# Optimization experiments

Measured on AMD Instinct MI355X. Metric: run time of the kernel, lower is better.

## Reference

```python
import jax, jax.numpy as jnp
import numpy as np

B, ENC_LEN, DEC_LEN = 4, 1024, 256
ENC_H, DEC_H, ATTN = 1024, 1024, 256


def setup_inputs() -> dict:
    key = jax.random.key(0)
    k1, k2, k3, k4, k5, k6 = jax.random.split(key, 6)
    scale = 0.02
    return {
        "encoded_seq": jax.random.normal(k1, (B, ENC_LEN, ENC_H), jnp.float32),
        "decoder_state": jax.random.normal(k2, (B, DEC_LEN, DEC_H), jnp.float32),
        "input_pad_mask": jnp.ones((B, ENC_LEN), jnp.float32),
        "Wh": jax.random.normal(k3, (ENC_H, ATTN), jnp.float32) * scale,
        "Ws": jax.random.normal(k4, (DEC_H, ATTN), jnp.float32) * scale,
        "bs": jax.random.normal(k5, (ATTN,), jnp.float32) * scale,
        "v": jax.random.normal(k6, (ATTN,), jnp.float32) * scale,
    }


def reference(encoded_seq, decoder_state, input_pad_mask, Wh, Ws, bs, v):
    # projections: [B, dec, A] and [B, enc, A]
    proj_dec = jnp.einsum('bdh,ha->bda', decoder_state, Ws) + bs
    proj_enc = jnp.einsum('beh,ha->bea', encoded_seq, Wh)
    # additive score: tanh(broadcast add) then dot with selector vector v
    added = jnp.tanh(proj_dec[:, :, None, :] + proj_enc[:, None, :, :])  # [B,dec,enc,A]
    attn_logits = jnp.einsum('bdea,a->bde', added, v)                    # [B,dec,enc]
    attn_weights = jax.nn.softmax(attn_logits, axis=-1)
    attn_weights2 = attn_weights * input_pad_mask[:, None, :]
    attn_renorm = attn_weights2 / jnp.sum(attn_weights2, axis=-1, keepdims=True)
    context = jnp.einsum('bde,beh->bdh', attn_renorm, encoded_seq)       # [B,dec,enc_h]
    return context, attn_renorm
```

## Files before the change

### kernel.cpp

```cpp
#include <hip/hip_runtime.h>
#include <hip/hip_bf16.h>

#define BB 4
#define ENC_LEN 1024
#define DEC_LEN 256
#define ENC_H 1024
#define ATTN_A 256

#define C2F 2.8853900817779268f

typedef short bf16x8 __attribute__((ext_vector_type(8)));
typedef float f32x4 __attribute__((ext_vector_type(4)));
typedef unsigned int u32x2 __attribute__((ext_vector_type(2)));

union Q2D {
  uint4 q;
  u32x2 d[2];
};
union BF8 {
  u32x2 d[2];
  bf16x8 v;
};

static __device__ __forceinline__ unsigned short f2bf(float x) {
  union {
    float f;
    unsigned int u;
  } c;
  c.f = x;
  unsigned int r = c.u + 0x7FFFu + ((c.u >> 16) & 1u);
  return (unsigned short)(r >> 16);
}

__global__ __launch_bounds__(256) void prep_k(
    const float* __restrict__ Wh, const float* __restrict__ Ws,
    const float* __restrict__ enc, const float* __restrict__ dec,
    unsigned short* __restrict__ WhT, unsigned short* __restrict__ WsT,
    unsigned short* __restrict__ encT, unsigned short* __restrict__ encB,
    unsigned short* __restrict__ decB) {
  __shared__ unsigned short T[64][68];
  const int wb = blockIdx.x;
  const int t = threadIdx.x;
  const int lr = t >> 4;
  const int lc4 = (t & 15) * 4;

  if (wb >= 1152) {
    const int q = wb - 1152;
    const int r0 = (q >> 4) * 64;
    const int c0 = (q & 15) * 64;
#pragma unroll
    for (int p = 0; p < 4; ++p) {
      const int r = lr + p * 16;
      const float4 v = *(const float4*)&dec[(long)(r0 + r) * ENC_H + c0 + lc4];
      ushort4 o;
      o.x = f2bf(v.x);
      o.y = f2bf(v.y);
      o.z = f2bf(v.z);
      o.w = f2bf(v.w);
      *(ushort4*)&decB[(long)(r0 + r) * ENC_H + c0 + lc4] = o;
    }
    return;
  }

  const float* in;
  unsigned short* out;
  unsigned short* out2 = nullptr;
  int R, C, bx, by;
  if (wb < 128) {
    in = (wb < 64) ? Wh : Ws;
    out = (wb < 64) ? WhT : WsT;
    const int tt = wb & 63;
    R = ENC_H;
    C = ATTN_A;
    bx = tt & 3;
    by = tt >> 2;
  } else {
    const int tt0 = wb - 128;
    const int b = tt0 >> 8;
    const int tt = tt0 & 255;
    in = enc + (long)b * ENC_LEN * ENC_H;
    out = encT + (long)b * ENC_H * ENC_LEN;
    out2 = encB + (long)b * ENC_LEN * ENC_H;
    R = ENC_LEN;
    C = ENC_H;
    bx = tt & 15;
    by = tt >> 4;
  }
  const int r0 = by * 64;
  const int c0 = bx * 64;

#pragma unroll
  for (int p = 0; p < 4; ++p) {
    const int r = lr + p * 16;
    const float4 v = *(const float4*)&in[(long)(r0 + r) * C + c0 + lc4];
    ushort4 o;
    o.x = f2bf(v.x);
    o.y = f2bf(v.y);
    o.z = f2bf(v.z);
    o.w = f2bf(v.w);
    *(ushort4*)&T[r][lc4] = o;
    if (out2) *(ushort4*)&out2[(long)(r0 + r) * C + c0 + lc4] = o;
  }
  __syncthreads();
#pragma unroll
  for (int p = 0; p < 4; ++p) {
    const int c = lr + p * 16;
    ushort4 o;
    o.x = T[lc4 + 0][c];
    o.y = T[lc4 + 1][c];
    o.z = T[lc4 + 2][c];
    o.w = T[lc4 + 3][c];
    *(ushort4*)&out[(long)(c0 + c) * R + r0 + lc4] = o;
  }
}

__global__ __launch_bounds__(256) void pgemm(const unsigned short* __restrict__ decB,
                                             const unsigned short* __restrict__ encB,
                                             const unsigned short* __restrict__ WsT,
                                             const unsigned short* __restrict__ WhT,
                                             float* __restrict__ pdP,
                                             float* __restrict__ peP) {
  __shared__ unsigned short As[64][36];
  __shared__ unsigned short Bs[64][36];
  __shared__ float Cs[64][68];

  const int s = blockIdx.z;
  const bool isPD = blockIdx.y < 16;
  const unsigned short* A = isPD ? decB : encB;
  const unsigned short* BT = isPD ? WsT : WhT;
  const int m0 = (isPD ? blockIdx.y : (blockIdx.y - 16)) * 64;
  const int n0 = blockIdx.x * 64;
  const int kb = s * 512;

  const int tid = threadIdx.x;
  const int lane = tid & 63;
  const int wave = tid >> 6;
  const int quad = lane >> 4;
  const int l16 = lane & 15;
  const int wm = (wave >> 1) * 32;
  const int wn = (wave & 1) * 32;
  const int sr = tid >> 2;
  const int sk = (tid & 3) * 8;

  f32x4 acc[2][2] = {{{0.f, 0.f, 0.f, 0.f}, {0.f, 0.f, 0.f, 0.f}},
                     {{0.f, 0.f, 0.f, 0.f}, {0.f, 0.f, 0.f, 0.f}}};

  const unsigned short* Ap = A + (long)(m0 + sr) * ENC_H + kb + sk;
  const unsigned short* Bp = BT + (long)(n0 + sr) * ENC_H + kb + sk;

  Q2D av, bv;
  av.q = *(const uint4*)(Ap);
  bv.q = *(const uint4*)(Bp);

  for (int k0 = 0; k0 < 512; k0 += 32) {
    __syncthreads();
    *(u32x2*)&As[sr][sk] = av.d[0];
    *(u32x2*)&As[sr][sk + 4] = av.d[1];
    *(u32x2*)&Bs[sr][sk] = bv.d[0];
    *(u32x2*)&Bs[sr][sk + 4] = bv.d[1];
    const int kn = (k0 + 32 < 512) ? (k0 + 32) : 0;
    av.q = *(const uint4*)(Ap + kn);
    bv.q = *(const uint4*)(Bp + kn);
    __syncthreads();

    bf16x8 af[2], bfr[2];
#pragma unroll
    for (int i = 0; i < 2; ++i) {
      BF8 t;
      t.d[0] = *(const u32x2*)&As[wm + i * 16 + l16][quad * 8];
      t.d[1] = *(const u32x2*)&As[wm + i * 16 + l16][quad * 8 + 4];
      af[i] = t.v;
    }
#pragma unroll
    for (int j = 0; j < 2; ++j) {
      BF8 t;
      t.d[0] = *(const u32x2*)&Bs[wn + j * 16 + l16][quad * 8];
      t.d[1] = *(const u32x2*)&Bs[wn + j * 16 + l16][quad * 8 + 4];
      bfr[j] = t.v;
    }
#pragma unroll
    for (int i = 0; i < 2; ++i)
#pragma unroll
      for (int j = 0; j < 2; ++j)
        acc[i][j] = __builtin_amdgcn_mfma_f32_16x16x32_bf16(af[i], bfr[j], acc[i][j],
                                                            0, 0, 0);
  }

  if (isPD) {
    float* out = pdP + (long)s * (1024 * ATTN_A);
#pragma unroll
    for (int j = 0; j < 2; ++j) {
      const int col = n0 + wn + j * 16 + l16;
#pragma unroll
      for (int i = 0; i < 2; ++i) {
        const int row = m0 + wm + i * 16 + quad * 4;
#pragma unroll
        for (int r = 0; r < 4; ++r)
          out[(long)(row + r) * ATTN_A + col] = C2F * acc[i][j][r];
      }
    }
  } else {
    __syncthreads();
#pragma unroll
    for (int i = 0; i < 2; ++i)
#pragma unroll
      for (int j = 0; j < 2; ++j)
#pragma unroll
        for (int r = 0; r < 4; ++r)
          Cs[wn + j * 16 + l16][wm + i * 16 + quad * 4 + r] = C2F * acc[i][j][r];
    __syncthreads();
    const int gb = m0 >> 10;
    const int e0 = m0 & 1023;
    float* out = peP + (long)s * (BB * ATTN_A * ENC_LEN);
#pragma unroll
    for (int p = 0; p < 4; ++p) {
      const int arow = (tid >> 4) + p * 16;
      const int e4 = (tid & 15) * 4;
      const float4 o = *(const float4*)&Cs[arow][e4];
      *(float4*)&out[(long)gb * (ATTN_A * ENC_LEN) + (long)(n0 + arow) * ENC_LEN +
                     e0 + e4] = o;
    }
  }
}

__global__ __launch_bounds__(256) void logits_k(const float* __restrict__ peP,
                                                const float* __restrict__ pdP,
                                                const float* __restrict__ v,
                                                const float* __restrict__ bs,
                                                float* __restrict__ p0,
                                                float* __restrict__ p1) {
  const int tid = threadIdx.x;
  const int e = blockIdx.x * 256 + tid;
  const int d0 = blockIdx.y * 8;
  const int b = blockIdx.z >> 1;
  const int a0 = (blockIdx.z & 1) * 128;

  __shared__ float Ed[128][8];
  __shared__ float vv[128];

  if (tid < 128) {
    const float cb = C2F * bs[a0 + tid];
#pragma unroll
    for (int dd = 0; dd < 8; ++dd) {
      const long idx = (long)(b * DEC_LEN + d0 + dd) * ATTN_A + a0 + tid;
      const float t = pdP[idx] + pdP[idx + 1024 * ATTN_A] + cb;
      Ed[tid][dd] = __builtin_amdgcn_exp2f(t);
    }
    vv[tid] = -2.0f * v[a0 + tid];
  }
  __syncthreads();

  float acc[8] = {0.f, 0.f, 0.f, 0.f, 0.f, 0.f, 0.f, 0.f};
  const float* pe0 = peP + (long)b * (ATTN_A * ENC_LEN) + (long)a0 * ENC_LEN + e;
  const float* pe1 = pe0 + (long)BB * ATTN_A * ENC_LEN;

  float pn0[4], pn1[4];
#pragma unroll
  for (int u = 0; u < 4; ++u) {
    pn0[u] = pe0[(long)u * ENC_LEN];
    pn1[u] = pe1[(long)u * ENC_LEN];
  }

  for (int a4 = 0; a4 < 128; a4 += 4) {
    float Ee[4];
#pragma unroll
    for (int u = 0; u < 4; ++u) Ee[u] = __builtin_amdgcn_exp2f(pn0[u] + pn1[u]);
    const int an = (a4 + 4 < 128) ? (a4 + 4) : 0;
#pragma unroll
    for (int u = 0; u < 4; ++u) {
      pn0[u] = pe0[(long)(an + u) * ENC_LEN];
      pn1[u] = pe1[(long)(an + u) * ENC_LEN];
    }
    const float4 v4 = *(const float4*)&vv[a4];

    float ed[4][8];
#pragma unroll
    for (int u = 0; u < 4; ++u) {
      const float4 e0v = *(const float4*)&Ed[a4 + u][0];
      const float4 e1v = *(const float4*)&Ed[a4 + u][4];
      ed[u][0] = e0v.x;
      ed[u][1] = e0v.y;
      ed[u][2] = e0v.z;
      ed[u][3] = e0v.w;
      ed[u][4] = e1v.x;
      ed[u][5] = e1v.y;
      ed[u][6] = e1v.z;
      ed[u][7] = e1v.w;
    }

#pragma unroll
    for (int dd = 0; dd < 8; ++dd) {
      const float dn0 = fmaf(ed[0][dd], Ee[0], 1.0f);
      const float dn1 = fmaf(ed[1][dd], Ee[1], 1.0f);
      const float dn2 = fmaf(ed[2][dd], Ee[2], 1.0f);
      const float dn3 = fmaf(ed[3][dd], Ee[3], 1.0f);
      const float x12 = dn0 * dn1;
      const float x34 = dn2 * dn3;
      float t1 = v4.x * dn1;
      t1 = fmaf(v4.y, dn0, t1);
      float t2 = v4.z * dn3;
      t2 = fmaf(v4.w, dn2, t2);
      float num = t1 * x34;
      num = fmaf(t2, x12, num);
      const float D = x12 * x34;
      const float r = __builtin_amdgcn_rcpf(D);
      acc[dd] = fmaf(num, r, acc[dd]);
    }
  }

  float* po = (blockIdx.z & 1) ? p1 : p0;
  const long base = ((long)(b * DEC_LEN + d0) * ENC_LEN) + e;
#pragma unroll
  for (int dd = 0; dd < 8; ++dd) po[base + (long)dd * ENC_LEN] = acc[dd];
}

__global__ __launch_bounds__(256) void softmax2_k(float* __restrict__ p0,
                                                  const float* __restrict__ p1,
                                                  const float* __restrict__ mask,
                                                  unsigned short* __restrict__ attnB) {
  const int row = blockIdx.x;
  const int b = row >> 8;
  const int tid = threadIdx.x;
  float* rp = p0 + (long)row * ENC_LEN;
  const float* rq = p1 + (long)row * ENC_LEN;
  const float* mp = mask + b * ENC_LEN;
  unsigned short* rb = attnB + (long)row * ENC_LEN;

  float l[4], m[4];
#pragma unroll
  for (int j = 0; j < 4; ++j) {
    l[j] = rp[tid + 256 * j] + rq[tid + 256 * j];
    m[j] = mp[tid + 256 * j];
  }

  __shared__ float redmax[4];
  __shared__ float redsum[4];
  const int lane = tid & 63;
  const int wid = tid >> 6;

  float tm = fmaxf(fmaxf(l[0], l[1]), fmaxf(l[2], l[3]));
#pragma unroll
  for (int off = 1; off < 64; off <<= 1) tm = fmaxf(tm, __shfl_xor(tm, off, 64));
  if (lane == 0) redmax[wid] = tm;
  __syncthreads();
  const float rmax = fmaxf(fmaxf(redmax[0], redmax[1]), fmaxf(redmax[2], redmax[3]));

  const float LOG2E = 1.4426950408889634f;
  float p[4];
  float ts = 0.f;
#pragma unroll
  for (int j = 0; j < 4; ++j) {
    p[j] = __builtin_amdgcn_exp2f((l[j] - rmax) * LOG2E) * m[j];
    ts += p[j];
  }
#pragma unroll
  for (int off = 1; off < 64; off <<= 1) ts += __shfl_xor(ts, off, 64);
  if (lane == 0) redsum[wid] = ts;
  __syncthreads();
  const float rsum = redsum[0] + redsum[1] + redsum[2] + redsum[3];

  const float inv = 1.0f / rsum;
#pragma unroll
  for (int j = 0; j < 4; ++j) {
    const float w = p[j] * inv;
    rp[tid + 256 * j] = w;
    rb[tid + 256 * j] = f2bf(w);
  }
}

__global__ __launch_bounds__(256) void cgemm(const unsigned short* __restrict__ attnB,
                                             const unsigned short* __restrict__ encT,
                                             float* __restrict__ cP) {
  __shared__ unsigned short As[64][36];
  __shared__ unsigned short Bs[64][36];

  const int b = blockIdx.z >> 1;
  const int s = blockIdx.z & 1;
  const int kb = s * 512;
  const unsigned short* A = attnB + (long)b * DEC_LEN * ENC_LEN;
  const unsigned short* BT = encT + (long)b * ENC_H * ENC_LEN;
  float* C = cP + (long)s * (BB * DEC_LEN * ENC_H) + (long)b * DEC_LEN * ENC_H;

  const int tid = threadIdx.x;
  const int lane = tid & 63;
  const int wave = tid >> 6;
  const int quad = lane >> 4;
  const int l16 = lane & 15;
  const int wm = (wave >> 1) * 32;
  const int wn = (wave & 1) * 32;
  const int m0 = blockIdx.y * 64;
  const int n0 = blockIdx.x * 64;
  const int sr = tid >> 2;
  const int sk = (tid & 3) * 8;

  f32x4 acc[2][2] = {{{0.f, 0.f, 0.f, 0.f}, {0.f, 0.f, 0.f, 0.f}},
                     {{0.f, 0.f, 0.f, 0.f}, {0.f, 0.f, 0.f, 0.f}}};

  const unsigned short* Ap = A + (long)(m0 + sr) * ENC_LEN + kb + sk;
  const unsigned short* Bp = BT + (long)(n0 + sr) * ENC_LEN + kb + sk;

  Q2D av, bv;
  av.q = *(const uint4*)(Ap);
  bv.q = *(const uint4*)(Bp);

  for (int k0 = 0; k0 < 512; k0 += 32) {
    __syncthreads();
    *(u32x2*)&As[sr][sk] = av.d[0];
    *(u32x2*)&As[sr][sk + 4] = av.d[1];
    *(u32x2*)&Bs[sr][sk] = bv.d[0];
    *(u32x2*)&Bs[sr][sk + 4] = bv.d[1];
    const int kn = (k0 + 32 < 512) ? (k0 + 32) : 0;
    av.q = *(const uint4*)(Ap + kn);
    bv.q = *(const uint4*)(Bp + kn);
    __syncthreads();

    bf16x8 af[2], bfr[2];
#pragma unroll
    for (int i = 0; i < 2; ++i) {
      BF8 t;
      t.d[0] = *(const u32x2*)&As[wm + i * 16 + l16][quad * 8];
      t.d[1] = *(const u32x2*)&As[wm + i * 16 + l16][quad * 8 + 4];
      af[i] = t.v;
    }
#pragma unroll
    for (int j = 0; j < 2; ++j) {
      BF8 t;
      t.d[0] = *(const u32x2*)&Bs[wn + j * 16 + l16][quad * 8];
      t.d[1] = *(const u32x2*)&Bs[wn + j * 16 + l16][quad * 8 + 4];
      bfr[j] = t.v;
    }
#pragma unroll
    for (int i = 0; i < 2; ++i)
#pragma unroll
      for (int j = 0; j < 2; ++j)
        acc[i][j] = __builtin_amdgcn_mfma_f32_16x16x32_bf16(af[i], bfr[j], acc[i][j],
                                                            0, 0, 0);
  }

#pragma unroll
  for (int j = 0; j < 2; ++j) {
    const int col = n0 + wn + j * 16 + l16;
#pragma unroll
    for (int i = 0; i < 2; ++i) {
      const int row = m0 + wm + i * 16 + quad * 4;
#pragma unroll
      for (int r = 0; r < 4; ++r) C[(long)(row + r) * ENC_H + col] = acc[i][j][r];
    }
  }
}

__global__ __launch_bounds__(256) void creduce(const float* __restrict__ cP,
                                               float* __restrict__ ctx) {
  const long i = ((long)blockIdx.x * 256 + threadIdx.x) * 4;
  const float4 x = *(const float4*)&cP[i];
  const float4 y = *(const float4*)&cP[i + (long)BB * DEC_LEN * ENC_H];
  float4 o;
  o.x = x.x + y.x;
  o.y = x.y + y.y;
  o.z = x.z + y.z;
  o.w = x.w + y.w;
  *(float4*)&ctx[i] = o;
}

template <int OMODE, bool BIAS>
__global__ __launch_bounds__(256) void gemm64(const float* __restrict__ A,
                                              const float* __restrict__ B,
                                              const float* __restrict__ bias,
                                              float* __restrict__ C,
                                              int K, int lda, int ldb, int ldc,
                                              long sA, long sB, long sC) {
  const int bz = blockIdx.z;
  A += (long)bz * sA;
  B += (long)bz * sB;
  C += (long)bz * sC;

  const int tid = threadIdx.x;
  const int tx = tid & 15;
  const int ty = tid >> 4;

  __shared__ float As2[16][64];
  __shared__ float Bs2[16][64];

  float acc[4][4];
#pragma unroll
  for (int i = 0; i < 4; ++i)
#pragma unroll
    for (int j = 0; j < 4; ++j) acc[i][j] = 0.f;

  const int ar = tid >> 2;
  const int ak4 = (tid & 3) << 2;
  const int br = tid >> 4;
  const int bn4 = (tid & 15) << 2;

  const float* Aload = A + (long)(blockIdx.y * 64 + ar) * lda + ak4;
  const float* Bload = B + (long)br * ldb + blockIdx.x * 64 + bn4;

  for (int k0 = 0; k0 < K; k0 += 16) {
    const float4 av = *(const float4*)(Aload + k0);
    const float4 bv = *(const float4*)(Bload + (long)k0 * ldb);
    __syncthreads();
    As2[ak4 + 0][ar] = av.x;
    As2[ak4 + 1][ar] = av.y;
    As2[ak4 + 2][ar] = av.z;
    As2[ak4 + 3][ar] = av.w;
    *(float4*)&Bs2[br][bn4] = bv;
    __syncthreads();
#pragma unroll
    for (int kk = 0; kk < 16; ++kk) {
      const float4 a4 = *(const float4*)&As2[kk][ty << 2];
      const float4 b4 = *(const float4*)&Bs2[kk][tx << 2];
      const float am[4] = {a4.x, a4.y, a4.z, a4.w};
      const float bn[4] = {b4.x, b4.y, b4.z, b4.w};
#pragma unroll
      for (int i = 0; i < 4; ++i)
#pragma unroll
        for (int j = 0; j < 4; ++j) acc[i][j] = fmaf(am[i], bn[j], acc[i][j]);
    }
  }

  if (OMODE == 0) {
    const int row0 = blockIdx.y * 64 + (ty << 2);
    const int col0 = blockIdx.x * 64 + (tx << 2);
    float4 bb4 = make_float4(0.f, 0.f, 0.f, 0.f);
    if (BIAS) bb4 = *(const float4*)&bias[col0];
#pragma unroll
    for (int i = 0; i < 4; ++i) {
      float4 o;
      o.x = acc[i][0] + bb4.x;
      o.y = acc[i][1] + bb4.y;
      o.z = acc[i][2] + bb4.z;
      o.w = acc[i][3] + bb4.w;
      *(float4*)&C[(long)(row0 + i) * ldc + col0] = o;
    }
  } else {
#pragma unroll
    for (int i = 0; i < 4; ++i) {
      const int gr = blockIdx.y * 64 + (ty << 2) + i;
      const int b = gr >> 10;
      const int e = gr & 1023;
#pragma unroll
      for (int j = 0; j < 4; ++j) {
        const int col = blockIdx.x * 64 + (tx << 2) + j;
        C[(long)b * (ATTN_A * ENC_LEN) + (long)col * ENC_LEN + e] = acc[i][j];
      }
    }
  }
}

__global__ __launch_bounds__(256) void logits_fb(const float* __restrict__ peT,
                                                 const float* __restrict__ pd,
                                                 const float* __restrict__ v,
                                                 float* __restrict__ out) {
  const int tid = threadIdx.x;
  const int e = blockIdx.x * 256 + tid;
  const int d0 = blockIdx.y * 8;
  const int b = blockIdx.z;

  __shared__ float cpd[ATTN_A][8];
  __shared__ float vv[ATTN_A];

  {
    const int a = tid;
#pragma unroll
    for (int dd = 0; dd < 8; ++dd)
      cpd[a][dd] = C2F * pd[((b * DEC_LEN + d0 + dd) * ATTN_A) + a];
    vv[a] = -2.0f * v[a];
  }
  __syncthreads();

  float acc[8] = {0.f, 0.f, 0.f, 0.f, 0.f, 0.f, 0.f, 0.f};
  const float* pe = peT + (long)b * (ATTN_A * ENC_LEN) + e;

  for (int a = 0; a < ATTN_A; a += 4) {
    float pes[4];
#pragma unroll
    for (int u = 0; u < 4; ++u) pes[u] = pe[(long)(a + u) * ENC_LEN];
#pragma unroll
    for (int u = 0; u < 4; ++u) {
      const float cpe = C2F * pes[u];
      const float vu = vv[a + u];
      const float4 c0 = *(const float4*)&cpd[a + u][0];
      const float4 c1 = *(const float4*)&cpd[a + u][4];
      const float cd[8] = {c0.x, c0.y, c0.z, c0.w, c1.x, c1.y, c1.z, c1.w};
#pragma unroll
      for (int dd = 0; dd < 8; ++dd) {
        const float x = cd[dd] + cpe;
        const float ex = __builtin_amdgcn_exp2f(x);
        const float r = __builtin_amdgcn_rcpf(ex + 1.0f);
        acc[dd] = fmaf(vu, r, acc[dd]);
      }
    }
  }

  const long base = ((long)(b * DEC_LEN + d0) * ENC_LEN) + e;
#pragma unroll
  for (int dd = 0; dd < 8; ++dd) out[base + (long)dd * ENC_LEN] = acc[dd];
}

__global__ __launch_bounds__(256) void softmax_fb(float* __restrict__ attn,
                                                  const float* __restrict__ mask) {
  const int row = blockIdx.x;
  const int b = row >> 8;
  const int tid = threadIdx.x;
  float* rp = attn + (long)row * ENC_LEN;
  const float* mp = mask + b * ENC_LEN;

  float l[4], m[4];
#pragma unroll
  for (int j = 0; j < 4; ++j) {
    l[j] = rp[tid + 256 * j];
    m[j] = mp[tid + 256 * j];
  }

  __shared__ float redmax[4];
  __shared__ float redsum[4];
  const int lane = tid & 63;
  const int wid = tid >> 6;

  float tm = fmaxf(fmaxf(l[0], l[1]), fmaxf(l[2], l[3]));
#pragma unroll
  for (int off = 1; off < 64; off <<= 1) tm = fmaxf(tm, __shfl_xor(tm, off, 64));
  if (lane == 0) redmax[wid] = tm;
  __syncthreads();
  const float rmax = fmaxf(fmaxf(redmax[0], redmax[1]), fmaxf(redmax[2], redmax[3]));

  const float LOG2E = 1.4426950408889634f;
  float p[4];
  float ts = 0.f;
#pragma unroll
  for (int j = 0; j < 4; ++j) {
    p[j] = __builtin_amdgcn_exp2f((l[j] - rmax) * LOG2E) * m[j];
    ts += p[j];
  }
#pragma unroll
  for (int off = 1; off < 64; off <<= 1) ts += __shfl_xor(ts, off, 64);
  if (lane == 0) redsum[wid] = ts;
  __syncthreads();
  const float rsum = redsum[0] + redsum[1] + redsum[2] + redsum[3];

  const float inv = 1.0f / rsum;
#pragma unroll
  for (int j = 0; j < 4; ++j) rp[tid + 256 * j] = p[j] * inv;
}

extern "C" void kernel_launch(void* const* d_in, const int* in_sizes, int n_in,
                              void* d_out, int out_size, void* d_ws, size_t ws_size,
                              hipStream_t stream) {
  const float* enc = (const float*)d_in[0];
  const float* dec = (const float*)d_in[1];
  const float* mask = (const float*)d_in[2];
  const float* Wh = (const float*)d_in[3];
  const float* Ws = (const float*)d_in[4];
  const float* bs = (const float*)d_in[5];
  const float* v = (const float*)d_in[6];

  float* ctx = (float*)d_out;
  float* attn = ctx + (long)BB * DEC_LEN * ENC_H;

  const long N_PD = 2L * 1024 * ATTN_A;
  const long N_PE = 2L * BB * ATTN_A * ENC_LEN;
  const long N_P1 = (long)BB * DEC_LEN * ENC_LEN;
  const long N_CP = 2L * BB * DEC_LEN * ENC_H;
  const long N_ENC = (long)BB * ENC_H * ENC_LEN;
  const long N_W = (long)ATTN_A * ENC_H;
  const long N_DEC = 1024L * ENC_H;
  const long N_ATT = (long)BB * DEC_LEN * ENC_LEN;
  const size_t FAST_WS = (N_PD + N_PE + N_P1 + N_CP) * 4 +
                         (N_ENC + 2 * N_W + N_ENC + N_DEC + N_ATT) * 2;

  if (ws_size >= FAST_WS) {
    float* pdP = (float*)d_ws;
    float* peP = pdP + N_PD;
    float* p1 = peP + N_PE;
    float* cP = p1 + N_P1;
    unsigned short* encT = (unsigned short*)(cP + N_CP);
    unsigned short* WhT = encT + N_ENC;
    unsigned short* WsT = WhT + N_W;
    unsigned short* encB = WsT + N_W;
    unsigned short* decB = encB + N_ENC;
    unsigned short* attnB = decB + N_DEC;

    prep_k<<<dim3(1408, 1, 1), 256, 0, stream>>>(Wh, Ws, enc, dec, WhT, WsT, encT,
                                                 encB, decB);
    pgemm<<<dim3(4, 80, 2), 256, 0, stream>>>(decB, encB, WsT, WhT, pdP, peP);
    logits_k<<<dim3(4, 32, BB * 2), 256, 0, stream>>>(peP, pdP, v, bs, attn, p1);
    softmax2_k<<<dim3(BB * DEC_LEN, 1, 1), 256, 0, stream>>>(attn, p1, mask, attnB);
    cgemm<<<dim3(16, 4, BB * 2), 256, 0, stream>>>(attnB, encT, cP);
    creduce<<<dim3(1024, 1, 1), 256, 0, stream>>>(cP, ctx);
  } else {
    float* pd = (float*)d_ws;
    float* peT = pd + (long)BB * DEC_LEN * ATTN_A;

    gemm64<0, true><<<dim3(ATTN_A / 64, (BB * DEC_LEN) / 64, 1), 256, 0, stream>>>(
        dec, Ws, bs, pd, ENC_H, ENC_H, ATTN_A, ATTN_A, 0, 0, 0);
    gemm64<1, false><<<dim3(ATTN_A / 64, (BB * ENC_LEN) / 64, 1), 256, 0, stream>>>(
        enc, Wh, nullptr, peT, ENC_H, ENC_H, ATTN_A, 0, 0, 0, 0);
    logits_fb<<<dim3(ENC_LEN / 256, DEC_LEN / 8, BB), 256, 0, stream>>>(peT, pd, v,
                                                                        attn);
    softmax_fb<<<dim3(BB * DEC_LEN, 1, 1), 256, 0, stream>>>(attn, mask);
    gemm64<0, false><<<dim3(ENC_H / 64, DEC_LEN / 64, BB), 256, 0, stream>>>(
        attn, enc, nullptr, ctx, ENC_LEN, ENC_LEN, ENC_H, ENC_H,
        (long)DEC_LEN * ENC_LEN, (long)ENC_LEN * ENC_H, (long)DEC_LEN * ENC_H);
  }
}
```

Before: 141.3 us.

## Drop split-K partials; fuse exp2 and bias into projection GEMM epilogue

The projection GEMM and the context GEMM no longer split K in two. This removes the partial-sum buffers, the creduce kernel and the extra partial read in softmax. The projection GEMM epilogue now applies the bias and exp2 directly and writes transposed enc exponentials straight from the MFMA layout, so logits_k no longer recomputes exp per (d, a) pair. logits_k now handles all 256 attention dims per block with an 8-way product-of-denominators trick, which means fewer rcp calls. The cost is fewer blocks (half the parallelism in both GEMMs) and longer K loops. The larger product of eight denominators also risks overflow.

```diff
diff --git a/kernel.cpp b/kernel.cpp
--- a/kernel.cpp
+++ b/kernel.cpp
@@ -118,19 +118,36 @@
                                              const unsigned short* __restrict__ encB,
                                              const unsigned short* __restrict__ WsT,
                                              const unsigned short* __restrict__ WhT,
-                                             float* __restrict__ pdP,
-                                             float* __restrict__ peP) {
+                                             const float* __restrict__ bs,
+                                             float* __restrict__ Ed,
+                                             float* __restrict__ Ee) {
   __shared__ unsigned short As[64][36];
   __shared__ unsigned short Bs[64][36];
-  __shared__ float Cs[64][68];
-
-  const int s = blockIdx.z;
-  const bool isPD = blockIdx.y < 16;
-  const unsigned short* A = isPD ? decB : encB;
-  const unsigned short* BT = isPD ? WsT : WhT;
-  const int m0 = (isPD ? blockIdx.y : (blockIdx.y - 16)) * 64;
-  const int n0 = blockIdx.x * 64;
-  const int kb = s * 512;
+
+  const int bid = blockIdx.x;
+  const bool isPD = bid < 64;
+  const unsigned short* A;
+  const unsigned short* BT;
+  float* out;
+  int ldc, m0, n0;
+  if (isPD) {
+    A = decB;
+    BT = WsT;
+    out = Ed;
+    ldc = ATTN_A;
+    m0 = (bid >> 2) * 64;
+    n0 = (bid & 3) * 64;
+  } else {
+    const int q = bid - 64;
+    const int b = q >> 6;
+    const int r = q & 63;
+    A = WhT;
+    BT = encB + (long)b * ENC_LEN * ENC_H;
+    out = Ee + (long)b * ATTN_A * ENC_LEN;
+    ldc = ENC_LEN;
+    m0 = (r >> 4) * 64;
+    n0 = (r & 15) * 64;
+  }
 
   const int tid = threadIdx.x;
   const int lane = tid & 63;
@@ -145,20 +162,20 @@
   f32x4 acc[2][2] = {{{0.f, 0.f, 0.f, 0.f}, {0.f, 0.f, 0.f, 0.f}},
                      {{0.f, 0.f, 0.f, 0.f}, {0.f, 0.f, 0.f, 0.f}}};
 
-  const unsigned short* Ap = A + (long)(m0 + sr) * ENC_H + kb + sk;
-  const unsigned short* Bp = BT + (long)(n0 + sr) * ENC_H + kb + sk;
+  const unsigned short* Ap = A + (long)(m0 + sr) * ENC_H + sk;
+  const unsigned short* Bp = BT + (long)(n0 + sr) * ENC_H + sk;
 
   Q2D av, bv;
   av.q = *(const uint4*)(Ap);
   bv.q = *(const uint4*)(Bp);
 
-  for (int k0 = 0; k0 < 512; k0 += 32) {
+  for (int k0 = 0; k0 < 1024; k0 += 32) {
     __syncthreads();
     *(u32x2*)&As[sr][sk] = av.d[0];
     *(u32x2*)&As[sr][sk + 4] = av.d[1];
     *(u32x2*)&Bs[sr][sk] = bv.d[0];
     *(u32x2*)&Bs[sr][sk + 4] = bv.d[1];
-    const int kn = (k0 + 32 < 512) ? (k0 + 32) : 0;
+    const int kn = (k0 + 32 < 1024) ? (k0 + 32) : 0;
     av.q = *(const uint4*)(Ap + kn);
     bv.q = *(const uint4*)(Bp + kn);
     __syncthreads();
@@ -186,150 +203,113 @@
                                                             0, 0, 0);
   }
 
-  if (isPD) {
-    float* out = pdP + (long)s * (1024 * ATTN_A);
-#pragma unroll
-    for (int j = 0; j < 2; ++j) {
-      const int col = n0 + wn + j * 16 + l16;
-#pragma unroll
-      for (int i = 0; i < 2; ++i) {
-        const int row = m0 + wm + i * 16 + quad * 4;
-#pragma unroll
-        for (int r = 0; r < 4; ++r)
-          out[(long)(row + r) * ATTN_A + col] = C2F * acc[i][j][r];
-      }
-    }
-  } else {
-    __syncthreads();
-#pragma unroll
-    for (int i = 0; i < 2; ++i)
-#pragma unroll
-      for (int j = 0; j < 2; ++j)
-#pragma unroll
-        for (int r = 0; r < 4; ++r)
-          Cs[wn + j * 16 + l16][wm + i * 16 + quad * 4 + r] = C2F * acc[i][j][r];
-    __syncthreads();
-    const int gb = m0 >> 10;
-    const int e0 = m0 & 1023;
-    float* out = peP + (long)s * (BB * ATTN_A * ENC_LEN);
-#pragma unroll
-    for (int p = 0; p < 4; ++p) {
-      const int arow = (tid >> 4) + p * 16;
-      const int e4 = (tid & 15) * 4;
-      const float4 o = *(const float4*)&Cs[arow][e4];
-      *(float4*)&out[(long)gb * (ATTN_A * ENC_LEN) + (long)(n0 + arow) * ENC_LEN +
-                     e0 + e4] = o;
-    }
-  }
-}
-
-__global__ __launch_bounds__(256) void logits_k(const float* __restrict__ peP,
-                                                const float* __restrict__ pdP,
+#pragma unroll
+  for (int j = 0; j < 2; ++j) {
+    const int col = n0 + wn + j * 16 + l16;
+    const float cb = isPD ? (C2F * bs[col]) : 0.f;
+#pragma unroll
+    for (int i = 0; i < 2; ++i) {
+      const int row = m0 + wm + i * 16 + quad * 4;
+#pragma unroll
+      for (int r = 0; r < 4; ++r)
+        out[(long)(row + r) * ldc + col] =
+            __builtin_amdgcn_exp2f(C2F * acc[i][j][r] + cb);
+    }
+  }
+}
+
+__global__ __launch_bounds__(256) void logits_k(const float* __restrict__ Ee,
+                                                const float* __restrict__ Ed,
                                                 const float* __restrict__ v,
-                                                const float* __restrict__ bs,
-                                                float* __restrict__ p0,
-                                                float* __restrict__ p1) {
+                                                float* __restrict__ p0) {
   const int tid = threadIdx.x;
   const int e = blockIdx.x * 256 + tid;
   const int d0 = blockIdx.y * 8;
-  const int b = blockIdx.z >> 1;
-  const int a0 = (blockIdx.z & 1) * 128;
-
-  __shared__ float Ed[128][8];
-  __shared__ float vv[128];
-
-  if (tid < 128) {
-    const float cb = C2F * bs[a0 + tid];
+  const int b = blockIdx.z;
+
+  __shared__ float Eds[8][256];
+  __shared__ float vv[256];
+
+#pragma unroll
+  for (int dd = 0; dd < 8; ++dd)
+    Eds[dd][tid] = Ed[(long)(b * DEC_LEN + d0 + dd) * ATTN_A + tid];
+  vv[tid] = -2.0f * v[tid];
+  __syncthreads();
+
+  float acc[8] = {0.f, 0.f, 0.f, 0.f, 0.f, 0.f, 0.f, 0.f};
+  const float* pe = Ee + (long)b * (ATTN_A * ENC_LEN) + e;
+
+  float pn[8];
+#pragma unroll
+  for (int u = 0; u < 8; ++u) pn[u] = pe[(long)u * ENC_LEN];
+
+  for (int a8 = 0; a8 < 256; a8 += 8) {
+    float ee[8];
+#pragma unroll
+    for (int u = 0; u < 8; ++u) ee[u] = pn[u];
+    const int an = (a8 + 8 < 256) ? (a8 + 8) : 0;
+#pragma unroll
+    for (int u = 0; u < 8; ++u) pn[u] = pe[(long)(an + u) * ENC_LEN];
+
+    const float4 v0 = *(const float4*)&vv[a8];
+    const float4 v1 = *(const float4*)&vv[a8 + 4];
+
 #pragma unroll
     for (int dd = 0; dd < 8; ++dd) {
-      const long idx = (long)(b * DEC_LEN + d0 + dd) * ATTN_A + a0 + tid;
-      const float t = pdP[idx] + pdP[idx + 1024 * ATTN_A] + cb;
-      Ed[tid][dd] = __builtin_amdgcn_exp2f(t);
-    }
-    vv[tid] = -2.0f * v[a0 + tid];
-  }
-  __syncthreads();
-
-  float acc[8] = {0.f, 0.f, 0.f, 0.f, 0.f, 0.f, 0.f, 0.f};
-  const float* pe0 = peP + (long)b * (ATTN_A * ENC_LEN) + (long)a0 * ENC_LEN + e;
-  const float* pe1 = pe0 + (long)BB * ATTN_A * ENC_LEN;
-
-  float pn0[4], pn1[4];
-#pragma unroll
-  for (int u = 0; u < 4; ++u) {
-    pn0[u] = pe0[(long)u * ENC_LEN];
-    pn1[u] = pe1[(long)u * ENC_LEN];
-  }
-
-  for (int a4 = 0; a4 < 128; a4 += 4) {
-    float Ee[4];
-#pragma unroll
-    for (int u = 0; u < 4; ++u) Ee[u] = __builtin_amdgcn_exp2f(pn0[u] + pn1[u]);
-    const int an = (a4 + 4 < 128) ? (a4 + 4) : 0;
-#pragma unroll
-    for (int u = 0; u < 4; ++u) {
-      pn0[u] = pe0[(long)(an + u) * ENC_LEN];
-      pn1[u] = pe1[(long)(an + u) * ENC_LEN];
-    }
-    const float4 v4 = *(const float4*)&vv[a4];
-
-    float ed[4][8];
-#pragma unroll
-    for (int u = 0; u < 4; ++u) {
-      const float4 e0v = *(const float4*)&Ed[a4 + u][0];
-      const float4 e1v = *(const float4*)&Ed[a4 + u][4];
-      ed[u][0] = e0v.x;
-      ed[u][1] = e0v.y;
-      ed[u][2] = e0v.z;
-      ed[u][3] = e0v.w;
-      ed[u][4] = e1v.x;
-      ed[u][5] = e1v.y;
-      ed[u][6] = e1v.z;
-      ed[u][7] = e1v.w;
-    }
-
-#pragma unroll
-    for (int dd = 0; dd < 8; ++dd) {
-      const float dn0 = fmaf(ed[0][dd], Ee[0], 1.0f);
-      const float dn1 = fmaf(ed[1][dd], Ee[1], 1.0f);
-      const float dn2 = fmaf(ed[2][dd], Ee[2], 1.0f);
-      const float dn3 = fmaf(ed[3][dd], Ee[3], 1.0f);
-      const float x12 = dn0 * dn1;
-      const float x34 = dn2 * dn3;
-      float t1 = v4.x * dn1;
-      t1 = fmaf(v4.y, dn0, t1);
-      float t2 = v4.z * dn3;
-      t2 = fmaf(v4.w, dn2, t2);
-      float num = t1 * x34;
-      num = fmaf(t2, x12, num);
-      const float D = x12 * x34;
-      const float r = __builtin_amdgcn_rcpf(D);
-      acc[dd] = fmaf(num, r, acc[dd]);
-    }
-  }
-
-  float* po = (blockIdx.z & 1) ? p1 : p0;
+      const float4 e0 = *(const float4*)&Eds[dd][a8];
+      const float4 e1 = *(const float4*)&Eds[dd][a8 + 4];
+      const float dn0 = fmaf(e0.x, ee[0], 1.0f);
+      const float dn1 = fmaf(e0.y, ee[1], 1.0f);
+      const float dn2 = fmaf(e0.z, ee[2], 1.0f);
+      const float dn3 = fmaf(e0.w, ee[3], 1.0f);
+      const float dn4 = fmaf(e1.x, ee[4], 1.0f);
+      const float dn5 = fmaf(e1.y, ee[5], 1.0f);
+      const float dn6 = fmaf(e1.z, ee[6], 1.0f);
+      const float dn7 = fmaf(e1.w, ee[7], 1.0f);
+      const float pA = dn0 * dn1;
+      const float pB = dn2 * dn3;
+      const float pC = dn4 * dn5;
+      const float pD = dn6 * dn7;
+      float sA = v0.x * dn1;
+      sA = fmaf(v0.y, dn0, sA);
+      float sB = v0.z * dn3;
+      sB = fmaf(v0.w, dn2, sB);
+      float sC = v1.x * dn5;
+      sC = fmaf(v1.y, dn4, sC);
+      float sD = v1.z * dn7;
+      sD = fmaf(v1.w, dn6, sD);
+      const float P1 = pA * pB;
+      const float P2 = pC * pD;
+      float S1 = sA * pB;
+      S1 = fmaf(sB, pA, S1);
+      float S2 = sC * pD;
+      S2 = fmaf(sD, pC, S2);
+      float num = S1 * P2;
+      num = fmaf(S2, P1, num);
+      const float D = P1 * P2;
+      acc[dd] = fmaf(num, __builtin_amdgcn_rcpf(D), acc[dd]);
+    }
+  }
+
   const long base = ((long)(b * DEC_LEN + d0) * ENC_LEN) + e;
 #pragma unroll
-  for (int dd = 0; dd < 8; ++dd) po[base + (long)dd * ENC_LEN] = acc[dd];
+  for (int dd = 0; dd < 8; ++dd) p0[base + (long)dd * ENC_LEN] = acc[dd];
 }
 
 __global__ __launch_bounds__(256) void softmax2_k(float* __restrict__ p0,
-                                                  const float* __restrict__ p1,
                                                   const float* __restrict__ mask,
                                                   unsigned short* __restrict__ attnB) {
   const int row = blockIdx.x;
   const int b = row >> 8;
   const int tid = threadIdx.x;
   float* rp = p0 + (long)row * ENC_LEN;
-  const float* rq = p1 + (long)row * ENC_LEN;
   const float* mp = mask + b * ENC_LEN;
   unsigned short* rb = attnB + (long)row * ENC_LEN;
 
   float l[4], m[4];
 #pragma unroll
   for (int j = 0; j < 4; ++j) {
-    l[j] = rp[tid + 256 * j] + rq[tid + 256 * j];
+    l[j] = rp[tid + 256 * j];
     m[j] = mp[tid + 256 * j];
   }
 
@@ -370,16 +350,14 @@
 
 __global__ __launch_bounds__(256) void cgemm(const unsigned short* __restrict__ attnB,
                                              const unsigned short* __restrict__ encT,
-                                             float* __restrict__ cP) {
+                                             float* __restrict__ ctx) {
   __shared__ unsigned short As[64][36];
   __shared__ unsigned short Bs[64][36];
 
-  const int b = blockIdx.z >> 1;
-  const int s = blockIdx.z & 1;
-  const int kb = s * 512;
+  const int b = blockIdx.z;
   const unsigned short* A = attnB + (long)b * DEC_LEN * ENC_LEN;
   const unsigned short* BT = encT + (long)b * ENC_H * ENC_LEN;
-  float* C = cP + (long)s * (BB * DEC_LEN * ENC_H) + (long)b * DEC_LEN * ENC_H;
+  float* C = ctx + (long)b * DEC_LEN * ENC_H;
 
   const int tid = threadIdx.x;
   const int lane = tid & 63;
@@ -396,20 +374,20 @@
   f32x4 acc[2][2] = {{{0.f, 0.f, 0.f, 0.f}, {0.f, 0.f, 0.f, 0.f}},
                      {{0.f, 0.f, 0.f, 0.f}, {0.f, 0.f, 0.f, 0.f}}};
 
-  const unsigned short* Ap = A + (long)(m0 + sr) * ENC_LEN + kb + sk;
-  const unsigned short* Bp = BT + (long)(n0 + sr) * ENC_LEN + kb + sk;
+  const unsigned short* Ap = A + (long)(m0 + sr) * ENC_LEN + sk;
+  const unsigned short* Bp = BT + (long)(n0 + sr) * ENC_LEN + sk;
 
   Q2D av, bv;
   av.q = *(const uint4*)(Ap);
   bv.q = *(const uint4*)(Bp);
 
-  for (int k0 = 0; k0 < 512; k0 += 32) {
+  for (int k0 = 0; k0 < 1024; k0 += 32) {
     __syncthreads();
     *(u32x2*)&As[sr][sk] = av.d[0];
     *(u32x2*)&As[sr][sk + 4] = av.d[1];
     *(u32x2*)&Bs[sr][sk] = bv.d[0];
     *(u32x2*)&Bs[sr][sk + 4] = bv.d[1];
-    const int kn = (k0 + 32 < 512) ? (k0 + 32) : 0;
+    const int kn = (k0 + 32 < 1024) ? (k0 + 32) : 0;
     av.q = *(const uint4*)(Ap + kn);
     bv.q = *(const uint4*)(Bp + kn);
     __syncthreads();
@@ -447,19 +425,6 @@
       for (int r = 0; r < 4; ++r) C[(long)(row + r) * ENC_H + col] = acc[i][j][r];
     }
   }
-}
-
-__global__ __launch_bounds__(256) void creduce(const float* __restrict__ cP,
-                                               float* __restrict__ ctx) {
-  const long i = ((long)blockIdx.x * 256 + threadIdx.x) * 4;
-  const float4 x = *(const float4*)&cP[i];
-  const float4 y = *(const float4*)&cP[i + (long)BB * DEC_LEN * ENC_H];
-  float4 o;
-  o.x = x.x + y.x;
-  o.y = x.y + y.y;
-  o.z = x.z + y.z;
-  o.w = x.w + y.w;
-  *(float4*)&ctx[i] = o;
 }
 
 template <int OMODE, bool BIAS>
@@ -657,23 +622,19 @@
   float* ctx = (float*)d_out;
   float* attn = ctx + (long)BB * DEC_LEN * ENC_H;
 
-  const long N_PD = 2L * 1024 * ATTN_A;
-  const long N_PE = 2L * BB * ATTN_A * ENC_LEN;
-  const long N_P1 = (long)BB * DEC_LEN * ENC_LEN;
-  const long N_CP = 2L * BB * DEC_LEN * ENC_H;
+  const long N_ED = 1024L * ATTN_A;
+  const long N_EE = (long)BB * ATTN_A * ENC_LEN;
   const long N_ENC = (long)BB * ENC_H * ENC_LEN;
   const long N_W = (long)ATTN_A * ENC_H;
   const long N_DEC = 1024L * ENC_H;
   const long N_ATT = (long)BB * DEC_LEN * ENC_LEN;
-  const size_t FAST_WS = (N_PD + N_PE + N_P1 + N_CP) * 4 +
-                         (N_ENC + 2 * N_W + N_ENC + N_DEC + N_ATT) * 2;
+  const size_t FAST_WS =
+      (N_ED + N_EE) * 4 + (N_ENC + 2 * N_W + N_ENC + N_DEC + N_ATT) * 2;
 
   if (ws_size >= FAST_WS) {
-    float* pdP = (float*)d_ws;
-    float* peP = pdP + N_PD;
-    float* p1 = peP + N_PE;
-    float* cP = p1 + N_P1;
-    unsigned short* encT = (unsigned short*)(cP + N_CP);
+    float* Ed = (float*)d_ws;
+    float* Ee = Ed + N_ED;
+    unsigned short* encT = (unsigned short*)(Ee + N_EE);
     unsigned short* WhT = encT + N_ENC;
     unsigned short* WsT = WhT + N_W;
     unsigned short* encB = WsT + N_W;
@@ -682,11 +643,10 @@
 
     prep_k<<<dim3(1408, 1, 1), 256, 0, stream>>>(Wh, Ws, enc, dec, WhT, WsT, encT,
                                                  encB, decB);
-    pgemm<<<dim3(4, 80, 2), 256, 0, stream>>>(decB, encB, WsT, WhT, pdP, peP);
-    logits_k<<<dim3(4, 32, BB * 2), 256, 0, stream>>>(peP, pdP, v, bs, attn, p1);
-    softmax2_k<<<dim3(BB * DEC_LEN, 1, 1), 256, 0, stream>>>(attn, p1, mask, attnB);
-    cgemm<<<dim3(16, 4, BB * 2), 256, 0, stream>>>(attnB, encT, cP);
-    creduce<<<dim3(1024, 1, 1), 256, 0, stream>>>(cP, ctx);
+    pgemm<<<dim3(320, 1, 1), 256, 0, stream>>>(decB, encB, WsT, WhT, bs, Ed, Ee);
+    logits_k<<<dim3(4, 32, BB), 256, 0, stream>>>(Ee, Ed, v, attn);
+    softmax2_k<<<dim3(BB * DEC_LEN, 1, 1), 256, 0, stream>>>(attn, mask, attnB);
+    cgemm<<<dim3(16, 4, BB), 256, 0, stream>>>(attnB, encT, ctx);
   } else {
     float* pd = (float*)d_ws;
     float* peT = pd + (long)BB * DEC_LEN * ATTN_A;
```

Result: no change. 142.3 us (+0.7%).
